# Optimization experiments

Hardware: AMD Instinct MI355X
Metric: run time of the kernel (lower is better)

The kernel has to match this reference:

```python
import jax, jax.numpy as jnp
import numpy as np

IN_F = 256
OUT_F = 256
ALPHA = 0.2  # LeakyReLU negative slope
NEG_INF = -9e15


def setup_inputs() -> dict:
    key = jax.random.key(0)
    k_h, k_adj, k_w, k_a = jax.random.split(key, 4)
    N = 8192
    h = jax.random.normal(k_h, (N, IN_F), dtype=jnp.float32)
    adj = jax.random.randint(k_adj, (N, N), 0, 2, dtype=jnp.int32)
    # xavier_uniform with gain=1.414
    gain = 1.414
    limW = gain * np.sqrt(6.0 / (IN_F + OUT_F))
    W = jax.random.uniform(k_w, (IN_F, OUT_F), minval=-limW, maxval=limW, dtype=jnp.float32)
    lima = gain * np.sqrt(6.0 / (2 * OUT_F + 1))
    a = jax.random.uniform(k_a, (2 * OUT_F, 1), minval=-lima, maxval=lima, dtype=jnp.float32)
    return {"h": h, "adj": adj, "W": W, "a": a}


def reference(h, adj, W, a):
    # Wh: [N, F]
    Wh = h @ W
    # The original materializes [N, N, 2F] concat pairs; equivalently
    # e[i, j] = leakyrelu(Wh[i] . a[:F] + Wh[j] . a[F:])
    a1 = a[:OUT_F, 0]  # [F]
    a2 = a[OUT_F:, 0]  # [F]
    s1 = Wh @ a1       # [N]
    s2 = Wh @ a2       # [N]
    e = jax.nn.leaky_relu(s1[:, None] + s2[None, :], negative_slope=ALPHA)  # [N, N]
    att = jnp.where(adj > 0, e, NEG_INF)
    att = jax.nn.softmax(att, axis=1)
    # dropout p=0.0 (eval) -> identity
    h_prime = att @ Wh  # [N, F]
    return jax.nn.elu(h_prime)  # concat=True path
```

## Files before the change

### kernel.cpp

```cpp
#include <hip/hip_runtime.h>

#define NN 8192
#define FF 256
#define PST 136

typedef _Float16 h8 __attribute__((ext_vector_type(8)));
typedef _Float16 h4 __attribute__((ext_vector_type(4)));
typedef float    f4 __attribute__((ext_vector_type(4)));
typedef int      i4v __attribute__((ext_vector_type(4)));

__device__ __forceinline__ unsigned fenc(float x) {
  unsigned u = __float_as_uint(x);
  return (u & 0x80000000u) ? ~u : (u | 0x80000000u);
}
__device__ __forceinline__ float fdec(unsigned e) {
  unsigned u = (e & 0x80000000u) ? (e ^ 0x80000000u) : ~e;
  return __uint_as_float(u);
}

__device__ __forceinline__ void sync_lds() {
  __builtin_amdgcn_s_waitcnt(0xc07f);
  __builtin_amdgcn_s_barrier();
}

__global__ __launch_bounds__(256) void k_wh(
    const float* __restrict__ h, const float* __restrict__ W,
    const float* __restrict__ a, _Float16* __restrict__ wfrag,
    float* __restrict__ s1, _Float16* __restrict__ s2h,
    unsigned* __restrict__ s2maxe) {
  __shared__ float hs[16 * 256];
  __shared__ _Float16 whs[16 * 264];
  __shared__ unsigned bm[4];
  const int t = threadIdx.x;
  const int r0 = blockIdx.x * 16;
#pragma unroll
  for (int i = 0; i < 4; ++i) {
    int idx = i * 1024 + t * 4;
    *(f4*)&hs[idx] = *(const f4*)&h[(size_t)r0 * 256 + idx];
  }
  __syncthreads();
  const int lane = t & 63;
  const int wv = t >> 6;
  const int rg = wv * 4;
  const int c4 = lane * 4;
  float acc[4][4];
#pragma unroll
  for (int i = 0; i < 4; ++i)
#pragma unroll
    for (int k = 0; k < 4; ++k) acc[i][k] = 0.f;
  f4 w[8];
#pragma unroll
  for (int i = 0; i < 8; ++i) w[i] = *(const f4*)&W[i * 256 + c4];
  for (int f = 0; f < 256; f += 8) {
    f4 nw[8];
    if (f < 248) {
#pragma unroll
      for (int i = 0; i < 8; ++i) nw[i] = *(const f4*)&W[(f + 8 + i) * 256 + c4];
    }
#pragma unroll
    for (int i = 0; i < 4; ++i) {
      f4 h0 = *(const f4*)&hs[(rg + i) * 256 + f];
      f4 h1 = *(const f4*)&hs[(rg + i) * 256 + f + 4];
#pragma unroll
      for (int k = 0; k < 4; ++k)
        acc[i][k] += h0[0]*w[0][k] + h0[1]*w[1][k] + h0[2]*w[2][k] + h0[3]*w[3][k]
                   + h1[0]*w[4][k] + h1[1]*w[5][k] + h1[2]*w[6][k] + h1[3]*w[7][k];
    }
    if (f < 248) {
#pragma unroll
      for (int i = 0; i < 8; ++i) w[i] = nw[i];
    }
  }
  float a1v[4], a2v[4];
#pragma unroll
  for (int k = 0; k < 4; ++k) { a1v[k] = a[c4 + k]; a2v[k] = a[256 + c4 + k]; }
  unsigned wmax = 0u;
#pragma unroll
  for (int i = 0; i < 4; ++i) {
    h4 hh;
    float p1 = 0.f, p2 = 0.f;
#pragma unroll
    for (int k = 0; k < 4; ++k) {
      hh[k] = (_Float16)acc[i][k];
      p1 += acc[i][k] * a1v[k];
      p2 += acc[i][k] * a2v[k];
    }
    *(h4*)&whs[(rg + i) * 264 + c4] = hh;
#pragma unroll
    for (int off = 32; off; off >>= 1) {
      p1 += __shfl_xor(p1, off);
      p2 += __shfl_xor(p2, off);
    }
    if (lane == 0) {
      const int r = r0 + rg + i;
      s1[r] = p1;
      s2h[r] = (_Float16)p2;
      const unsigned e = fenc(p2);
      wmax = (e > wmax) ? e : wmax;
    }
  }
  if (lane == 0) bm[wv] = wmax;
  __syncthreads();
  if (t == 0) {
    unsigned m01 = (bm[0] > bm[1]) ? bm[0] : bm[1];
    unsigned m23 = (bm[2] > bm[3]) ? bm[2] : bm[3];
    atomicMax(s2maxe, (m01 > m23) ? m01 : m23);
  }
  {
    const int kt = blockIdx.x >> 1;
    const int hb = blockIdx.x & 1;
    const int lp = hb * 32 + (t & 31);
    const int kb = ((t & 31) >> 4) * 8;
    const int m16e = t & 15;
#pragma unroll
    for (int p = 0; p < 2; ++p) {
      const int n = (t >> 5) + p * 8;
      h8 v;
#pragma unroll
      for (int j = 0; j < 8; ++j) v[j] = whs[(kb + j) * 264 + n * 16 + m16e];
      *(h8*)&wfrag[(((size_t)kt * 16 + n) << 9) + lp * 8] = v;
    }
  }
}

__global__ __launch_bounds__(512, 4) void k_gat(
    const int* __restrict__ adj, const _Float16* __restrict__ wfrag,
    const float* __restrict__ s1g, const _Float16* __restrict__ s2h,
    const unsigned* __restrict__ s2maxe,
    float* __restrict__ o0, float* __restrict__ o1,
    float* __restrict__ o2, float* __restrict__ o3,
    float* __restrict__ lbuf) {
  __shared__ _Float16 P[2][64 * PST];
  __shared__ _Float16 s2l[2048];
  const int t = threadIdx.x;
  const int lane = t & 63;
  const int w = t >> 6;
  const int q = lane >> 4;
  const int m16 = lane & 15;
  const int rt = (int)blockIdx.x >> 2;
  const int kq = (int)blockIdx.x & 3;
  const int r0 = rt * 64;

  if (t < 256) ((h8*)s2l)[t] = ((const h8*)(s2h + kq * 2048))[t];

  const int srA = 8 * w + q;
  const int srB = srA + 4;
  const float s2m = fdec(*s2maxe);
  const float s1A = s1g[r0 + srA];
  const float s1B = s1g[r0 + srB];
  const float uA0 = s1A + s2m, uB0 = s1B + s2m;
  const float miA = fmaxf(uA0, 0.2f * uA0);
  const float miB = fmaxf(uB0, 0.2f * uB0);
  const float sAmi = s1A - miA, sBmi = s1B - miB;

  f4 acc[4][2];
#pragma unroll
  for (int m = 0; m < 4; ++m)
#pragma unroll
    for (int n = 0; n < 2; ++n)
#pragma unroll
      for (int e = 0; e < 4; ++e) acc[m][n][e] = 0.f;
  float lsA = 0.f, lsB = 0.f;

  const int* adjA = adj + (size_t)(r0 + srA) * NN + kq * 2048 + m16 * 8;
  const int* adjB = adj + (size_t)(r0 + srB) * NN + kq * 2048 + m16 * 8;
  __syncthreads();

  i4v a0 = *(const i4v*)(adjA);
  i4v a1 = *(const i4v*)(adjA + 4);
  i4v b0 = *(const i4v*)(adjB);
  i4v b1 = *(const i4v*)(adjB + 4);

  for (int p = 0; p < 16; ++p) {
    const _Float16* wfb =
        wfrag + ((((size_t)(kq * 64 + p * 4)) * 16 + 2 * w) << 9) + lane * 8;
    h8 bb[8];
#pragma unroll
    for (int ks = 0; ks < 4; ++ks) {
      bb[2 * ks]     = *(const h8*)(wfb + ks * 8192);
      bb[2 * ks + 1] = *(const h8*)(wfb + ks * 8192 + 512);
    }
    i4v na0 = a0, na1 = a1, nb0 = b0, nb1 = b1;
    if (p < 15) {
      na0 = *(const i4v*)(adjA + (p + 1) * 128);
      na1 = *(const i4v*)(adjA + (p + 1) * 128 + 4);
      nb0 = *(const i4v*)(adjB + (p + 1) * 128);
      nb1 = *(const i4v*)(adjB + (p + 1) * 128 + 4);
    }
    const h8 s2c = *(const h8*)&s2l[p * 128 + m16 * 8];
    h8 pA, pB;
#pragma unroll
    for (int j = 0; j < 8; ++j) {
      const float s2v = (float)s2c[j];
      const int mA = (j < 4) ? a0[j] : a1[j - 4];
      const int mB = (j < 4) ? b0[j] : b1[j - 4];
      const float uA = s1A + s2v;
      const float uB = s1B + s2v;
      const float argA = sAmi + s2v - 0.8f * fminf(uA, 0.f);
      const float argB = sBmi + s2v - 0.8f * fminf(uB, 0.f);
      const float pvA = (mA > 0) ? __expf(argA) : 0.f;
      const float pvB = (mB > 0) ? __expf(argB) : 0.f;
      lsA += pvA; pA[j] = (_Float16)pvA;
      lsB += pvB; pB[j] = (_Float16)pvB;
    }
    _Float16* Pb = &P[p & 1][0];
    *(h8*)&Pb[srA * PST + m16 * 8] = pA;
    *(h8*)&Pb[srB * PST + m16 * 8] = pB;
    sync_lds();
#pragma unroll
    for (int ks = 0; ks < 4; ++ks) {
      const h8 A0 = *(const h8*)&Pb[(     m16) * PST + ks * 32 + q * 8];
      const h8 A1 = *(const h8*)&Pb[(16 + m16) * PST + ks * 32 + q * 8];
      const h8 A2 = *(const h8*)&Pb[(32 + m16) * PST + ks * 32 + q * 8];
      const h8 A3 = *(const h8*)&Pb[(48 + m16) * PST + ks * 32 + q * 8];
      acc[0][0] = __builtin_amdgcn_mfma_f32_16x16x32_f16(A0, bb[2*ks],   acc[0][0], 0, 0, 0);
      acc[0][1] = __builtin_amdgcn_mfma_f32_16x16x32_f16(A0, bb[2*ks+1], acc[0][1], 0, 0, 0);
      acc[1][0] = __builtin_amdgcn_mfma_f32_16x16x32_f16(A1, bb[2*ks],   acc[1][0], 0, 0, 0);
      acc[1][1] = __builtin_amdgcn_mfma_f32_16x16x32_f16(A1, bb[2*ks+1], acc[1][1], 0, 0, 0);
      acc[2][0] = __builtin_amdgcn_mfma_f32_16x16x32_f16(A2, bb[2*ks],   acc[2][0], 0, 0, 0);
      acc[2][1] = __builtin_amdgcn_mfma_f32_16x16x32_f16(A2, bb[2*ks+1], acc[2][1], 0, 0, 0);
      acc[3][0] = __builtin_amdgcn_mfma_f32_16x16x32_f16(A3, bb[2*ks],   acc[3][0], 0, 0, 0);
      acc[3][1] = __builtin_amdgcn_mfma_f32_16x16x32_f16(A3, bb[2*ks+1], acc[3][1], 0, 0, 0);
    }
    a0 = na0; a1 = na1; b0 = nb0; b1 = nb1;
  }

  lsA += __shfl_xor(lsA, 1);
  lsA += __shfl_xor(lsA, 2);
  lsA += __shfl_xor(lsA, 4);
  lsA += __shfl_xor(lsA, 8);
  lsB += __shfl_xor(lsB, 1);
  lsB += __shfl_xor(lsB, 2);
  lsB += __shfl_xor(lsB, 4);
  lsB += __shfl_xor(lsB, 8);
  if (m16 == 0) {
    lbuf[kq * NN + r0 + srA] = lsA;
    lbuf[kq * NN + r0 + srB] = lsB;
  }

  float* ob = (kq == 0) ? o0 : (kq == 1) ? o1 : (kq == 2) ? o2 : o3;
#pragma unroll
  for (int m = 0; m < 4; ++m)
#pragma unroll
    for (int n = 0; n < 2; ++n)
#pragma unroll
      for (int v = 0; v < 4; ++v)
        ob[(size_t)(r0 + m * 16 + q * 4 + v) * FF + w * 32 + n * 16 + m16] =
            acc[m][n][v];
}

__global__ __launch_bounds__(256) void k_fin(
    float* __restrict__ out, const float* __restrict__ o1,
    const float* __restrict__ o2, const float* __restrict__ o3,
    const float* __restrict__ lbuf) {
  const int t = threadIdx.x;
  const int row = blockIdx.x * 16 + (t >> 4);
  const int c0 = (t & 15) * 16;
  const float linv = 1.0f / (lbuf[row] + lbuf[NN + row] +
                             lbuf[2 * NN + row] + lbuf[3 * NN + row]);
#pragma unroll
  for (int i = 0; i < 4; ++i) {
    f4 v0 = *(const f4*)&out[(size_t)row * FF + c0 + i * 4];
    f4 v1 = *(const f4*)&o1[(size_t)row * FF + c0 + i * 4];
    f4 v2 = *(const f4*)&o2[(size_t)row * FF + c0 + i * 4];
    f4 v3 = *(const f4*)&o3[(size_t)row * FF + c0 + i * 4];
    f4 o;
#pragma unroll
    for (int e = 0; e < 4; ++e) {
      float x = (v0[e] + v1[e] + v2[e] + v3[e]) * linv;
      o[e] = (x > 0.f) ? x : (__expf(x) - 1.f);
    }
    *(f4*)&out[(size_t)row * FF + c0 + i * 4] = o;
  }
}

extern "C" void kernel_launch(void* const* d_in, const int* in_sizes, int n_in,
                              void* d_out, int out_size, void* d_ws, size_t ws_size,
                              hipStream_t stream) {
  const float* h   = (const float*)d_in[0];
  const int*   adj = (const int*)d_in[1];
  const float* W   = (const float*)d_in[2];
  const float* a   = (const float*)d_in[3];
  float* out = (float*)d_out;

  char* ws = (char*)d_ws;
  _Float16* wfrag = (_Float16*)ws;
  float*    o1    = (float*)(ws + (4u << 20));
  float*    o2    = (float*)(ws + (12u << 20));
  float*    o3    = (float*)(ws + (20u << 20));
  float*    lbuf  = (float*)(ws + (28u << 20));
  unsigned* s2me  = (unsigned*)(ws + (28u << 20) + 131072);
  float*    s1    = (float*)(ws + (28u << 20) + 131072 + 64);
  _Float16* s2h   = (_Float16*)(ws + (28u << 20) + 131072 + 64 + 32768);

  hipMemsetAsync(s2me, 0, 4, stream);
  k_wh<<<512, 256, 0, stream>>>(h, W, a, wfrag, s1, s2h, s2me);
  k_gat<<<512, 512, 0, stream>>>(adj, wfrag, s1, s2h, s2me, out, o1, o2, o3, lbuf);
  k_fin<<<512, 256, 0, stream>>>(out, o1, o2, o3, lbuf);
}
```

Baseline: 417.5 us.

## Software-pipeline attention-probability compute one stage ahead of MFMA accumulation

Restructures the main loop so the exp/mask computation for tile p+1 is written into the alternate LDS buffer while MFMAs consume tile p. The adjacency prefetch distance grows to two tiles. The intent is to overlap VALU exp work with matrix-core work and hide global-load latency behind it. In exchange it needs more registers, which may lower occupancy, and it depends on the double-buffer barrier placement being correct.

New measurement: 423.6 us. No clear change (+1.5%).

```diff
diff --git a/kernel.cpp b/kernel.cpp
--- a/kernel.cpp
+++ b/kernel.cpp
@@ -166,34 +166,22 @@
   const int* adjB = adj + (size_t)(r0 + srB) * NN + kq * 2048 + m16 * 8;
   __syncthreads();
 
-  i4v a0 = *(const i4v*)(adjA);
-  i4v a1 = *(const i4v*)(adjA + 4);
-  i4v b0 = *(const i4v*)(adjB);
-  i4v b1 = *(const i4v*)(adjB + 4);
-
-  for (int p = 0; p < 16; ++p) {
-    const _Float16* wfb =
-        wfrag + ((((size_t)(kq * 64 + p * 4)) * 16 + 2 * w) << 9) + lane * 8;
-    h8 bb[8];
-#pragma unroll
-    for (int ks = 0; ks < 4; ++ks) {
-      bb[2 * ks]     = *(const h8*)(wfb + ks * 8192);
-      bb[2 * ks + 1] = *(const h8*)(wfb + ks * 8192 + 512);
-    }
-    i4v na0 = a0, na1 = a1, nb0 = b0, nb1 = b1;
-    if (p < 15) {
-      na0 = *(const i4v*)(adjA + (p + 1) * 128);
-      na1 = *(const i4v*)(adjA + (p + 1) * 128 + 4);
-      nb0 = *(const i4v*)(adjB + (p + 1) * 128);
-      nb1 = *(const i4v*)(adjB + (p + 1) * 128 + 4);
-    }
-    const h8 s2c = *(const h8*)&s2l[p * 128 + m16 * 8];
+  i4v g0a0 = *(const i4v*)(adjA);
+  i4v g0a1 = *(const i4v*)(adjA + 4);
+  i4v g0b0 = *(const i4v*)(adjB);
+  i4v g0b1 = *(const i4v*)(adjB + 4);
+  i4v cNa0 = *(const i4v*)(adjA + 128);
+  i4v cNa1 = *(const i4v*)(adjA + 132);
+  i4v cNb0 = *(const i4v*)(adjB + 128);
+  i4v cNb1 = *(const i4v*)(adjB + 132);
+  {
+    const h8 s2c = *(const h8*)&s2l[m16 * 8];
     h8 pA, pB;
 #pragma unroll
     for (int j = 0; j < 8; ++j) {
       const float s2v = (float)s2c[j];
-      const int mA = (j < 4) ? a0[j] : a1[j - 4];
-      const int mB = (j < 4) ? b0[j] : b1[j - 4];
+      const int mA = (j < 4) ? g0a0[j] : g0a1[j - 4];
+      const int mB = (j < 4) ? g0b0[j] : g0b1[j - 4];
       const float uA = s1A + s2v;
       const float uB = s1B + s2v;
       const float argA = sAmi + s2v - 0.8f * fminf(uA, 0.f);
@@ -203,10 +191,50 @@
       lsA += pvA; pA[j] = (_Float16)pvA;
       lsB += pvB; pB[j] = (_Float16)pvB;
     }
+    _Float16* Pw = &P[0][0];
+    *(h8*)&Pw[srA * PST + m16 * 8] = pA;
+    *(h8*)&Pw[srB * PST + m16 * 8] = pB;
+  }
+  sync_lds();
+
+  for (int p = 0; p < 16; ++p) {
+    const _Float16* wfb =
+        wfrag + ((((size_t)(kq * 64 + p * 4)) * 16 + 2 * w) << 9) + lane * 8;
+    h8 bb[8];
+#pragma unroll
+    for (int ks = 0; ks < 4; ++ks) {
+      bb[2 * ks]     = *(const h8*)(wfb + ks * 8192);
+      bb[2 * ks + 1] = *(const h8*)(wfb + ks * 8192 + 512);
+    }
+    i4v fa0 = cNa0, fa1 = cNa1, fb0 = cNb0, fb1 = cNb1;
+    if (p < 14) {
+      fa0 = *(const i4v*)(adjA + (p + 2) * 128);
+      fa1 = *(const i4v*)(adjA + (p + 2) * 128 + 4);
+      fb0 = *(const i4v*)(adjB + (p + 2) * 128);
+      fb1 = *(const i4v*)(adjB + (p + 2) * 128 + 4);
+    }
+    if (p < 15) {
+      const h8 s2c = *(const h8*)&s2l[(p + 1) * 128 + m16 * 8];
+      h8 pA, pB;
+#pragma unroll
+      for (int j = 0; j < 8; ++j) {
+        const float s2v = (float)s2c[j];
+        const int mA = (j < 4) ? cNa0[j] : cNa1[j - 4];
+        const int mB = (j < 4) ? cNb0[j] : cNb1[j - 4];
+        const float uA = s1A + s2v;
+        const float uB = s1B + s2v;
+        const float argA = sAmi + s2v - 0.8f * fminf(uA, 0.f);
+        const float argB = sBmi + s2v - 0.8f * fminf(uB, 0.f);
+        const float pvA = (mA > 0) ? __expf(argA) : 0.f;
+        const float pvB = (mB > 0) ? __expf(argB) : 0.f;
+        lsA += pvA; pA[j] = (_Float16)pvA;
+        lsB += pvB; pB[j] = (_Float16)pvB;
+      }
+      _Float16* Pw = &P[(p + 1) & 1][0];
+      *(h8*)&Pw[srA * PST + m16 * 8] = pA;
+      *(h8*)&Pw[srB * PST + m16 * 8] = pB;
+    }
     _Float16* Pb = &P[p & 1][0];
-    *(h8*)&Pb[srA * PST + m16 * 8] = pA;
-    *(h8*)&Pb[srB * PST + m16 * 8] = pB;
-    sync_lds();
 #pragma unroll
     for (int ks = 0; ks < 4; ++ks) {
       const h8 A0 = *(const h8*)&Pb[(     m16) * PST + ks * 32 + q * 8];
@@ -222,7 +250,8 @@
       acc[3][0] = __builtin_amdgcn_mfma_f32_16x16x32_f16(A3, bb[2*ks],   acc[3][0], 0, 0, 0);
       acc[3][1] = __builtin_amdgcn_mfma_f32_16x16x32_f16(A3, bb[2*ks+1], acc[3][1], 0, 0, 0);
     }
-    a0 = na0; a1 = na1; b0 = nb0; b1 = nb1;
+    sync_lds();
+    cNa0 = fa0; cNa1 = fa1; cNb0 = fb0; cNb1 = fb1;
   }
 
   lsA += __shfl_xor(lsA, 1);
```
